# Optimization experiments

Measured on AMD Instinct MI355X. Metric: run time of the kernel, lower is better.

The kernel has to match this reference:

```python
import jax, jax.numpy as jnp
import jax.scipy.fft as jsp_fft
import numpy as np

B, NX, NY, DV = 4, 512, 512, 32
KX, KY = 64, 64


def setup_inputs() -> dict:
    key = jax.random.key(0)
    k1, k2, k3 = jax.random.split(key, 3)
    x = jax.random.normal(k1, (B, NX, NY, DV), dtype=jnp.float32)
    R_real = jax.random.uniform(k2, (DV, DV, KX, KY), dtype=jnp.float32)
    R_imag = jax.random.uniform(k3, (DV, DV, KX, KY), dtype=jnp.float32)
    return {"x": x, "R_real": R_real, "R_imag": R_imag}


def reference(x, R_real, R_imag):
    # x: [B, nX, nY, dv]
    R = R_real + 1j * R_imag  # [dv_out, dv_in, kX, kY]
    kX, kY = R.shape[-2:]
    nX = x.shape[1]

    xt = jnp.moveaxis(x, -1, -3)                      # [B, dv, nX, nY]
    xd = jsp_fft.dct(xt, type=2, axis=-1, norm='ortho')   # DCT-II along Y
    xf = jnp.fft.rfft(xd, axis=-2, norm='ortho')      # [B, dv, nX//2+1, nY] complex
    nXf, nY = xf.shape[-2:]

    # Truncation einsum with identity-padded T matrices == slicing
    xtr = xf[..., :kX, :kY]                           # [B, dv, kX, kY]
    # Per-mode complex channel mixing
    y = jnp.einsum('ijab,ejab->eiab', R, xtr)         # [B, dv, kX, kY]
    # Inverse truncation == zero-padding back to full spectrum
    yp = jnp.pad(y, ((0, 0), (0, 0), (0, nXf - kX), (0, nY - kY)))

    yr = jnp.fft.irfft(yp, n=nX, axis=-2, norm='ortho')
    yd = jsp_fft.idct(yr, type=2, axis=-1, norm='ortho')
    return jnp.moveaxis(yd, -3, -1)                   # [B, nX, nY, dv]
```

## Files before the change

kernel.cpp:

```cpp
#include <hip/hip_runtime.h>
#include <math.h>

#define BB 4
#define NXD 512
#define NYD 512
#define DVD 32
#define KXD 64
#define KYD 64

#define OFF_DN  0
#define OFF_DT  32768
#define OFF_FCN 65536
#define OFF_FSN 98304
#define OFF_FCT 131072
#define OFF_FST 163840
#define OFF_C   196608
#define OFF_FR  4390912
#define OFF_FI  4915200
#define OFF_YR  5439488
#define OFF_YI  5963776
#define OFF_G   6488064

__global__ __launch_bounds__(256) void k_tables(float* __restrict__ ws) {
    int idx = blockIdx.x * 256 + threadIdx.x;
    int k = idx >> 9;
    int n = idx & 511;
    const float inv_sq512 = 0.04419417382415922f;
    float ak = (k == 0) ? inv_sq512 : 0.0625f;
    int m = (k * (2 * n + 1)) & 2047;
    float d = ak * cospif((float)m * (1.0f / 1024.0f));
    ws[OFF_DN + k * 512 + n] = d;
    ws[OFF_DT + n * 64 + k] = d;
    int mf = (k * n) & 511;
    float c = cospif((float)mf * (1.0f / 256.0f)) * inv_sq512;
    float s = sinpif((float)mf * (1.0f / 256.0f)) * inv_sq512;
    ws[OFF_FCN + k * 512 + n] = c;
    ws[OFF_FSN + k * 512 + n] = s;
    ws[OFF_FCT + n * 64 + k] = c;
    ws[OFF_FST + n * 64 + k] = s;
}

__global__ __launch_bounds__(256) void k_dct(const float* __restrict__ x,
                                             const float* __restrict__ ws,
                                             float* __restrict__ C) {
    __shared__ __align__(16) float xs[2][64 * 32];
    __shared__ __align__(16) float dt[64 * 64];
    int b = blockIdx.x >> 8;
    int nx = (blockIdx.x & 255) * 2;
    int t = threadIdx.x;
    int dv0 = (t & 15) * 2;
    int ky0 = (t >> 4) * 4;
    const float* Dt = ws + OFF_DT;
    float a[2][4][2] = {};
    for (int ch = 0; ch < 8; ++ch) {
        int ny0 = ch * 64;
        __syncthreads();
#pragma unroll
        for (int n = 0; n < 2; ++n) {
            const float4* src = (const float4*)(x + ((size_t)(b * NXD + nx + n) * NYD + ny0) * DVD);
            float4* dst = (float4*)xs[n];
#pragma unroll
            for (int p = 0; p < 2; ++p) dst[p * 256 + t] = src[p * 256 + t];
        }
        {
            const float4* src = (const float4*)(Dt + ny0 * 64);
            float4* dst = (float4*)dt;
#pragma unroll
            for (int p = 0; p < 4; ++p) dst[p * 256 + t] = src[p * 256 + t];
        }
        __syncthreads();
#pragma unroll 4
        for (int nyc = 0; nyc < 64; ++nyc) {
            float4 d4 = *(const float4*)(dt + nyc * 64 + ky0);
            float2 x0 = *(const float2*)(xs[0] + nyc * 32 + dv0);
            float2 x1 = *(const float2*)(xs[1] + nyc * 32 + dv0);
            float da[4] = {d4.x, d4.y, d4.z, d4.w};
#pragma unroll
            for (int q = 0; q < 4; ++q) {
                a[0][q][0] += da[q] * x0.x; a[0][q][1] += da[q] * x0.y;
                a[1][q][0] += da[q] * x1.x; a[1][q][1] += da[q] * x1.y;
            }
        }
    }
#pragma unroll
    for (int n = 0; n < 2; ++n)
#pragma unroll
        for (int q = 0; q < 4; ++q) {
            float2 v; v.x = a[n][q][0]; v.y = a[n][q][1];
            *(float2*)(C + ((size_t)((b * KYD + ky0 + q) * NXD + nx + n)) * DVD + dv0) = v;
        }
}

__global__ __launch_bounds__(256) void k_rfft(const float* __restrict__ Cbuf,
                                              const float* __restrict__ ws,
                                              float* __restrict__ Fr,
                                              float* __restrict__ Fi) {
    __shared__ __align__(16) float cs[256 * 16];
    int b = blockIdx.x >> 7;
    int r = blockIdx.x & 127;
    int ky = r >> 1;
    int dvbase = (r & 1) * 16;
    int t = threadIdx.x;
    int dv0 = (t & 7) * 2;
    int kx0 = (t >> 3) * 2;
    const float* Tc = ws + OFF_FCT;
    const float* Ts = ws + OFF_FST;
    float ar[2][2] = {}, ai[2][2] = {};
    for (int ch = 0; ch < 2; ++ch) {
        int nx0 = ch * 256;
        __syncthreads();
#pragma unroll
        for (int p = 0; p < 4; ++p) {
            int fi4 = p * 256 + t;
            int row = fi4 >> 2, c4 = fi4 & 3;
            *(float4*)(cs + row * 16 + c4 * 4) =
                *(const float4*)(Cbuf + ((size_t)(b * KYD + ky) * NXD + nx0 + row) * DVD + dvbase + c4 * 4);
        }
        __syncthreads();
#pragma unroll 4
        for (int nxc = 0; nxc < 256; ++nxc) {
            float2 cv = *(const float2*)(cs + nxc * 16 + dv0);
            float2 c2 = *(const float2*)(Tc + (nx0 + nxc) * 64 + kx0);
            float2 s2 = *(const float2*)(Ts + (nx0 + nxc) * 64 + kx0);
            ar[0][0] += c2.x * cv.x; ar[0][1] += c2.x * cv.y;
            ar[1][0] += c2.y * cv.x; ar[1][1] += c2.y * cv.y;
            ai[0][0] -= s2.x * cv.x; ai[0][1] -= s2.x * cv.y;
            ai[1][0] -= s2.y * cv.x; ai[1][1] -= s2.y * cv.y;
        }
    }
#pragma unroll
    for (int q = 0; q < 2; ++q) {
        size_t o = ((size_t)((b * KYD + ky) * KXD + kx0 + q)) * DVD + dvbase + dv0;
        float2 vr; vr.x = ar[q][0]; vr.y = ar[q][1];
        float2 vi; vi.x = ai[q][0]; vi.y = ai[q][1];
        *(float2*)(Fr + o) = vr;
        *(float2*)(Fi + o) = vi;
    }
}

__global__ __launch_bounds__(256) void k_mix(const float* __restrict__ Rr,
                                             const float* __restrict__ Ri,
                                             const float* __restrict__ Fr,
                                             const float* __restrict__ Fi,
                                             float* __restrict__ Yr,
                                             float* __restrict__ Yi) {
    __shared__ float fl[4 * 32 * 64 * 2];
    int kx = blockIdx.x & 63;
    int ig = blockIdx.x >> 6;
    int t = threadIdx.x;
    int j = t & 31, kyb = t >> 5;
#pragma unroll
    for (int e = 0; e < 4; ++e) {
#pragma unroll
        for (int p = 0; p < 8; ++p) {
            int ky = p * 8 + kyb;
            size_t go = ((size_t)((e * KYD + ky) * KXD + kx)) * DVD + j;
            int lo = ((e * 32 + j) * 64 + ((ky + j) & 63)) * 2;
            fl[lo] = Fr[go];
            fl[lo + 1] = Fi[go];
        }
    }
    __syncthreads();
    int lane = t & 63, w = t >> 6;
    int i = ig * 4 + w;
    float yr[4] = {}, yi[4] = {};
    for (int jj = 0; jj < 32; ++jj) {
        float rr = Rr[(((size_t)i * 32 + jj) * 64 + kx) * 64 + lane];
        float ri = Ri[(((size_t)i * 32 + jj) * 64 + kx) * 64 + lane];
#pragma unroll
        for (int e = 0; e < 4; ++e) {
            float2 f = *(const float2*)(fl + ((e * 32 + jj) * 64 + ((lane + jj) & 63)) * 2);
            yr[e] += rr * f.x - ri * f.y;
            yi[e] += rr * f.y + ri * f.x;
        }
    }
#pragma unroll
    for (int e = 0; e < 4; ++e) {
        size_t o = ((size_t)((e * DVD + i) * KXD + kx)) * KYD + lane;
        Yr[o] = yr[e];
        Yi[o] = yi[e];
    }
}

__global__ __launch_bounds__(256) void k_irfft(const float* __restrict__ Yr,
                                               const float* __restrict__ Yi,
                                               const float* __restrict__ ws,
                                               float* __restrict__ G) {
    __shared__ __align__(16) float ylr[64 * 64];
    __shared__ __align__(16) float yli[64 * 64];
    int blk = blockIdx.x;
    int oct = blk & 7;
    int i = (blk >> 3) & 31;
    int b = blk >> 8;
    int t = threadIdx.x;
    size_t ybase = ((size_t)(b * DVD + i)) * KXD * KYD;
#pragma unroll
    for (int p = 0; p < 16; ++p) {
        int idx = p * 256 + t;
        float wk = (idx < 64) ? 1.0f : 2.0f;
        ylr[idx] = Yr[ybase + idx] * wk;
        yli[idx] = Yi[ybase + idx] * wk;
    }
    __syncthreads();
    int kyg = t & 15, nxg = t >> 4;
    int ky0 = kyg * 4;
    int gnx0 = oct * 64 + nxg * 4;
    const float* Tc = ws + OFF_FCN;
    const float* Ts = ws + OFF_FSN;
    float acc[4][4] = {};
    for (int kx = 0; kx < 64; ++kx) {
        float4 cv = *(const float4*)(Tc + kx * 512 + gnx0);
        float4 sv = *(const float4*)(Ts + kx * 512 + gnx0);
        float4 vr = *(const float4*)(ylr + kx * 64 + ky0);
        float4 vi = *(const float4*)(yli + kx * 64 + ky0);
        float ca[4] = {cv.x, cv.y, cv.z, cv.w};
        float sa[4] = {sv.x, sv.y, sv.z, sv.w};
        float ra[4] = {vr.x, vr.y, vr.z, vr.w};
        float ia[4] = {vi.x, vi.y, vi.z, vi.w};
#pragma unroll
        for (int q = 0; q < 4; ++q)
#pragma unroll
            for (int kk = 0; kk < 4; ++kk)
                acc[q][kk] += ca[q] * ra[kk] - sa[q] * ia[kk];
    }
#pragma unroll
    for (int q = 0; q < 4; ++q) {
        float4 v; v.x = acc[q][0]; v.y = acc[q][1]; v.z = acc[q][2]; v.w = acc[q][3];
        *(float4*)(G + (((size_t)(b * NXD + gnx0 + q)) * DVD + i) * KYD + ky0) = v;
    }
}

#define GST 68
__global__ __launch_bounds__(256) void k_idct(const float* __restrict__ G,
                                              const float* __restrict__ ws,
                                              float* __restrict__ out) {
    __shared__ __align__(16) float gs[2][32 * GST];
    __shared__ __align__(16) float dn[64 * 64];
    int b = blockIdx.x >> 8;
    int nx = (blockIdx.x & 255) * 2;
    int t = threadIdx.x;
    int ig = t & 15, nyg = t >> 4;
    int i0 = ig * 2;
    const float* Dn = ws + OFF_DN;
#pragma unroll
    for (int n = 0; n < 2; ++n) {
        const float4* src = (const float4*)(G + (size_t)(b * NXD + nx + n) * DVD * KYD);
#pragma unroll
        for (int p = 0; p < 2; ++p) {
            int f = p * 256 + t;
            int i = f >> 4, ky4 = (f & 15) * 4;
            *(float4*)(gs[n] + i * GST + ky4) = src[f];
        }
    }
    float* outb = out + ((size_t)(b * NXD + nx)) * NYD * DVD;
    for (int c = 0; c < 8; ++c) {
        __syncthreads();
        {
            float4* dst = (float4*)dn;
#pragma unroll
            for (int p = 0; p < 4; ++p) {
                int f = p * 256 + t;
                int ky = f >> 4, ny4 = (f & 15) * 4;
                dst[f] = *(const float4*)(Dn + ky * 512 + c * 64 + ny4);
            }
        }
        __syncthreads();
        float acc[2][4][2] = {};
#pragma unroll 2
        for (int kyc = 0; kyc < 16; ++kyc) {
            int ky0 = kyc * 4;
            float4 g00 = *(const float4*)(gs[0] + i0 * GST + ky0);
            float4 g01 = *(const float4*)(gs[0] + (i0 + 1) * GST + ky0);
            float4 g10 = *(const float4*)(gs[1] + i0 * GST + ky0);
            float4 g11 = *(const float4*)(gs[1] + (i0 + 1) * GST + ky0);
            float g0a[2][4] = {{g00.x, g00.y, g00.z, g00.w}, {g10.x, g10.y, g10.z, g10.w}};
            float g1a[2][4] = {{g01.x, g01.y, g01.z, g01.w}, {g11.x, g11.y, g11.z, g11.w}};
#pragma unroll
            for (int kk = 0; kk < 4; ++kk) {
                float4 dv = *(const float4*)(dn + (ky0 + kk) * 64 + nyg * 4);
                float da[4] = {dv.x, dv.y, dv.z, dv.w};
#pragma unroll
                for (int q = 0; q < 4; ++q) {
                    acc[0][q][0] += da[q] * g0a[0][kk];
                    acc[0][q][1] += da[q] * g1a[0][kk];
                    acc[1][q][0] += da[q] * g0a[1][kk];
                    acc[1][q][1] += da[q] * g1a[1][kk];
                }
            }
        }
        int ny0 = c * 64 + nyg * 4;
#pragma unroll
        for (int n = 0; n < 2; ++n)
#pragma unroll
            for (int q = 0; q < 4; ++q) {
                float2 v; v.x = acc[n][q][0]; v.y = acc[n][q][1];
                *(float2*)(outb + ((size_t)n * NYD + ny0 + q) * DVD + i0) = v;
            }
    }
}

extern "C" void kernel_launch(void* const* d_in, const int* in_sizes, int n_in,
                              void* d_out, int out_size, void* d_ws, size_t ws_size,
                              hipStream_t stream) {
    const float* x  = (const float*)d_in[0];
    const float* Rr = (const float*)d_in[1];
    const float* Ri = (const float*)d_in[2];
    float* out = (float*)d_out;
    float* ws  = (float*)d_ws;
    float* C   = ws + OFF_C;
    float* Fr  = ws + OFF_FR;
    float* Fi  = ws + OFF_FI;
    float* Yr  = ws + OFF_YR;
    float* Yi  = ws + OFF_YI;
    float* G   = ws + OFF_G;

    k_tables<<<128, 256, 0, stream>>>(ws);
    k_dct<<<BB * (NXD / 2), 256, 0, stream>>>(x, ws, C);
    k_rfft<<<BB * KYD * 2, 256, 0, stream>>>(C, ws, Fr, Fi);
    k_mix<<<KXD * 8, 256, 0, stream>>>(Rr, Ri, Fr, Fi, Yr, Yi);
    k_irfft<<<BB * DVD * 8, 256, 0, stream>>>(Yr, Yi, ws, G);
    k_idct<<<BB * NXD / 2, 256, 0, stream>>>(G, ws, out);
}
```

Before: 432.1 us.

## Double-buffer DCT/rFFT staging with direct global-to-LDS loads and retune other kernels

In the DCT and rFFT kernels, x and C tiles are now staged into shared memory with direct global-to-LDS loads into two buffers, so the next chunk loads while the current one is computed. The DCT and iDCT kernels also stop copying the cosine tables into shared memory and read them straight from global memory (cache). The mixing kernel is split across twice as many blocks, each handling two batches, to raise parallelism. The irFFT kernel loads its input with float4 accesses. The risks are more global or cache traffic for the table reads, twice the R reads in the mixing kernel, and correctness of the asynchronous LDS loads without explicit waits beyond the barriers.

After: 469.3 us. 1.09x slower.

```diff
diff --git a/kernel.cpp b/kernel.cpp
--- a/kernel.cpp
+++ b/kernel.cpp
@@ -20,6 +20,12 @@
 #define OFF_YR  5439488
 #define OFF_YI  5963776
 #define OFF_G   6488064
+
+__device__ __forceinline__ void gload_lds16(const float* g, float* l) {
+    __builtin_amdgcn_global_load_lds(
+        (const __attribute__((address_space(1))) void*)g,
+        (__attribute__((address_space(3))) void*)l, 16, 0, 0);
+}
 
 __global__ __launch_bounds__(256) void k_tables(float* __restrict__ ws) {
     int idx = blockIdx.x * 256 + threadIdx.x;
@@ -43,37 +49,41 @@
 __global__ __launch_bounds__(256) void k_dct(const float* __restrict__ x,
                                              const float* __restrict__ ws,
                                              float* __restrict__ C) {
-    __shared__ __align__(16) float xs[2][64 * 32];
-    __shared__ __align__(16) float dt[64 * 64];
+    __shared__ __align__(16) float xs[2][2 * 2048];
     int b = blockIdx.x >> 8;
     int nx = (blockIdx.x & 255) * 2;
     int t = threadIdx.x;
+    int wv = t >> 6;
     int dv0 = (t & 15) * 2;
     int ky0 = (t >> 4) * 4;
     const float* Dt = ws + OFF_DT;
+    const float* xb = x + (size_t)(b * NXD + nx) * NYD * DVD;
+
+    auto stage = [&](int buf, int ch) {
+#pragma unroll
+        for (int n = 0; n < 2; ++n) {
+            const float* src = xb + ((size_t)n * NYD + ch * 64) * DVD;
+#pragma unroll
+            for (int p = 0; p < 2; ++p) {
+                int f = p * 256 + t;
+                gload_lds16(src + f * 4, xs[buf] + n * 2048 + (p * 256 + wv * 64) * 4);
+            }
+        }
+    };
+
     float a[2][4][2] = {};
+    stage(0, 0);
+    __syncthreads();
     for (int ch = 0; ch < 8; ++ch) {
-        int ny0 = ch * 64;
-        __syncthreads();
-#pragma unroll
-        for (int n = 0; n < 2; ++n) {
-            const float4* src = (const float4*)(x + ((size_t)(b * NXD + nx + n) * NYD + ny0) * DVD);
-            float4* dst = (float4*)xs[n];
-#pragma unroll
-            for (int p = 0; p < 2; ++p) dst[p * 256 + t] = src[p * 256 + t];
-        }
-        {
-            const float4* src = (const float4*)(Dt + ny0 * 64);
-            float4* dst = (float4*)dt;
-#pragma unroll
-            for (int p = 0; p < 4; ++p) dst[p * 256 + t] = src[p * 256 + t];
-        }
-        __syncthreads();
+        int buf = ch & 1;
+        if (ch < 7) stage(buf ^ 1, ch + 1);
+        const float* dtc = Dt + ch * 4096 + ky0;
+        const float* xsb = xs[buf];
 #pragma unroll 4
         for (int nyc = 0; nyc < 64; ++nyc) {
-            float4 d4 = *(const float4*)(dt + nyc * 64 + ky0);
-            float2 x0 = *(const float2*)(xs[0] + nyc * 32 + dv0);
-            float2 x1 = *(const float2*)(xs[1] + nyc * 32 + dv0);
+            float4 d4 = *(const float4*)(dtc + nyc * 64);
+            float2 x0 = *(const float2*)(xsb + nyc * 32 + dv0);
+            float2 x1 = *(const float2*)(xsb + 2048 + nyc * 32 + dv0);
             float da[4] = {d4.x, d4.y, d4.z, d4.w};
 #pragma unroll
             for (int q = 0; q < 4; ++q) {
@@ -81,6 +91,7 @@
                 a[1][q][0] += da[q] * x1.x; a[1][q][1] += da[q] * x1.y;
             }
         }
+        __syncthreads();
     }
 #pragma unroll
     for (int n = 0; n < 2; ++n)
@@ -95,31 +106,39 @@
                                               const float* __restrict__ ws,
                                               float* __restrict__ Fr,
                                               float* __restrict__ Fi) {
-    __shared__ __align__(16) float cs[256 * 16];
+    __shared__ __align__(16) float cs[2][4096];
     int b = blockIdx.x >> 7;
     int r = blockIdx.x & 127;
     int ky = r >> 1;
     int dvbase = (r & 1) * 16;
     int t = threadIdx.x;
+    int wv = t >> 6;
     int dv0 = (t & 7) * 2;
     int kx0 = (t >> 3) * 2;
     const float* Tc = ws + OFF_FCT;
     const float* Ts = ws + OFF_FST;
-    float ar[2][2] = {}, ai[2][2] = {};
-    for (int ch = 0; ch < 2; ++ch) {
-        int nx0 = ch * 256;
-        __syncthreads();
+    const float* Cb = Cbuf + (size_t)(b * KYD + ky) * NXD * DVD + dvbase;
+
+    auto stage = [&](int buf, int ch) {
 #pragma unroll
         for (int p = 0; p < 4; ++p) {
             int fi4 = p * 256 + t;
             int row = fi4 >> 2, c4 = fi4 & 3;
-            *(float4*)(cs + row * 16 + c4 * 4) =
-                *(const float4*)(Cbuf + ((size_t)(b * KYD + ky) * NXD + nx0 + row) * DVD + dvbase + c4 * 4);
-        }
-        __syncthreads();
-#pragma unroll 4
+            gload_lds16(Cb + (size_t)(ch * 256 + row) * DVD + c4 * 4,
+                        cs[buf] + (p * 256 + wv * 64) * 4);
+        }
+    };
+
+    float ar[2][2] = {}, ai[2][2] = {};
+    stage(0, 0);
+    __syncthreads();
+    for (int ch = 0; ch < 2; ++ch) {
+        if (ch == 0) stage(1, 1);
+        const float* csb = cs[ch];
+        int nx0 = ch * 256;
+#pragma unroll 8
         for (int nxc = 0; nxc < 256; ++nxc) {
-            float2 cv = *(const float2*)(cs + nxc * 16 + dv0);
+            float2 cv = *(const float2*)(csb + nxc * 16 + dv0);
             float2 c2 = *(const float2*)(Tc + (nx0 + nxc) * 64 + kx0);
             float2 s2 = *(const float2*)(Ts + (nx0 + nxc) * 64 + kx0);
             ar[0][0] += c2.x * cv.x; ar[0][1] += c2.x * cv.y;
@@ -127,6 +146,7 @@
             ai[0][0] -= s2.x * cv.x; ai[0][1] -= s2.x * cv.y;
             ai[1][0] -= s2.y * cv.x; ai[1][1] -= s2.y * cv.y;
         }
+        __syncthreads();
     }
 #pragma unroll
     for (int q = 0; q < 2; ++q) {
@@ -144,18 +164,20 @@
                                              const float* __restrict__ Fi,
                                              float* __restrict__ Yr,
                                              float* __restrict__ Yi) {
-    __shared__ float fl[4 * 32 * 64 * 2];
+    __shared__ float fl[2 * 32 * 64 * 2];
     int kx = blockIdx.x & 63;
-    int ig = blockIdx.x >> 6;
+    int ig = (blockIdx.x >> 6) & 7;
+    int eh = blockIdx.x >> 9;
     int t = threadIdx.x;
     int j = t & 31, kyb = t >> 5;
 #pragma unroll
-    for (int e = 0; e < 4; ++e) {
+    for (int e2 = 0; e2 < 2; ++e2) {
+        int e = eh * 2 + e2;
 #pragma unroll
         for (int p = 0; p < 8; ++p) {
             int ky = p * 8 + kyb;
             size_t go = ((size_t)((e * KYD + ky) * KXD + kx)) * DVD + j;
-            int lo = ((e * 32 + j) * 64 + ((ky + j) & 63)) * 2;
+            int lo = ((e2 * 32 + j) * 64 + ((ky + j) & 63)) * 2;
             fl[lo] = Fr[go];
             fl[lo + 1] = Fi[go];
         }
@@ -163,22 +185,25 @@
     __syncthreads();
     int lane = t & 63, w = t >> 6;
     int i = ig * 4 + w;
-    float yr[4] = {}, yi[4] = {};
+    size_t rb = (size_t)(i * 32) * 4096 + kx * 64 + lane;
+    float yr[2] = {}, yi[2] = {};
+#pragma unroll 8
     for (int jj = 0; jj < 32; ++jj) {
-        float rr = Rr[(((size_t)i * 32 + jj) * 64 + kx) * 64 + lane];
-        float ri = Ri[(((size_t)i * 32 + jj) * 64 + kx) * 64 + lane];
-#pragma unroll
-        for (int e = 0; e < 4; ++e) {
-            float2 f = *(const float2*)(fl + ((e * 32 + jj) * 64 + ((lane + jj) & 63)) * 2);
-            yr[e] += rr * f.x - ri * f.y;
-            yi[e] += rr * f.y + ri * f.x;
-        }
-    }
-#pragma unroll
-    for (int e = 0; e < 4; ++e) {
+        float rr = Rr[rb + (size_t)jj * 4096];
+        float ri = Ri[rb + (size_t)jj * 4096];
+#pragma unroll
+        for (int e2 = 0; e2 < 2; ++e2) {
+            float2 f = *(const float2*)(fl + ((e2 * 32 + jj) * 64 + ((lane + jj) & 63)) * 2);
+            yr[e2] += rr * f.x - ri * f.y;
+            yi[e2] += rr * f.y + ri * f.x;
+        }
+    }
+#pragma unroll
+    for (int e2 = 0; e2 < 2; ++e2) {
+        int e = eh * 2 + e2;
         size_t o = ((size_t)((e * DVD + i) * KXD + kx)) * KYD + lane;
-        Yr[o] = yr[e];
-        Yi[o] = yi[e];
+        Yr[o] = yr[e2];
+        Yi[o] = yi[e2];
     }
 }
 
@@ -195,11 +220,15 @@
     int t = threadIdx.x;
     size_t ybase = ((size_t)(b * DVD + i)) * KXD * KYD;
 #pragma unroll
-    for (int p = 0; p < 16; ++p) {
-        int idx = p * 256 + t;
-        float wk = (idx < 64) ? 1.0f : 2.0f;
-        ylr[idx] = Yr[ybase + idx] * wk;
-        yli[idx] = Yi[ybase + idx] * wk;
+    for (int p = 0; p < 4; ++p) {
+        int f = p * 256 + t;
+        float wk = (f < 16) ? 1.0f : 2.0f;
+        float4 vr = *(const float4*)(Yr + ybase + (size_t)f * 4);
+        float4 vi = *(const float4*)(Yi + ybase + (size_t)f * 4);
+        vr.x *= wk; vr.y *= wk; vr.z *= wk; vr.w *= wk;
+        vi.x *= wk; vi.y *= wk; vi.z *= wk; vi.w *= wk;
+        *(float4*)(ylr + f * 4) = vr;
+        *(float4*)(yli + f * 4) = vi;
     }
     __syncthreads();
     int kyg = t & 15, nxg = t >> 4;
@@ -235,7 +264,6 @@
                                               const float* __restrict__ ws,
                                               float* __restrict__ out) {
     __shared__ __align__(16) float gs[2][32 * GST];
-    __shared__ __align__(16) float dn[64 * 64];
     int b = blockIdx.x >> 8;
     int nx = (blockIdx.x & 255) * 2;
     int t = threadIdx.x;
@@ -252,19 +280,10 @@
             *(float4*)(gs[n] + i * GST + ky4) = src[f];
         }
     }
+    __syncthreads();
     float* outb = out + ((size_t)(b * NXD + nx)) * NYD * DVD;
     for (int c = 0; c < 8; ++c) {
-        __syncthreads();
-        {
-            float4* dst = (float4*)dn;
-#pragma unroll
-            for (int p = 0; p < 4; ++p) {
-                int f = p * 256 + t;
-                int ky = f >> 4, ny4 = (f & 15) * 4;
-                dst[f] = *(const float4*)(Dn + ky * 512 + c * 64 + ny4);
-            }
-        }
-        __syncthreads();
+        const float* dnc = Dn + c * 64 + nyg * 4;
         float acc[2][4][2] = {};
 #pragma unroll 2
         for (int kyc = 0; kyc < 16; ++kyc) {
@@ -277,7 +296,7 @@
             float g1a[2][4] = {{g01.x, g01.y, g01.z, g01.w}, {g11.x, g11.y, g11.z, g11.w}};
 #pragma unroll
             for (int kk = 0; kk < 4; ++kk) {
-                float4 dv = *(const float4*)(dn + (ky0 + kk) * 64 + nyg * 4);
+                float4 dv = *(const float4*)(dnc + (ky0 + kk) * 512);
                 float da[4] = {dv.x, dv.y, dv.z, dv.w};
 #pragma unroll
                 for (int q = 0; q < 4; ++q) {
@@ -317,7 +336,7 @@
     k_tables<<<128, 256, 0, stream>>>(ws);
     k_dct<<<BB * (NXD / 2), 256, 0, stream>>>(x, ws, C);
     k_rfft<<<BB * KYD * 2, 256, 0, stream>>>(C, ws, Fr, Fi);
-    k_mix<<<KXD * 8, 256, 0, stream>>>(Rr, Ri, Fr, Fi, Yr, Yi);
+    k_mix<<<KXD * 8 * 2, 256, 0, stream>>>(Rr, Ri, Fr, Fi, Yr, Yi);
     k_irfft<<<BB * DVD * 8, 256, 0, stream>>>(Yr, Yi, ws, G);
     k_idct<<<BB * NXD / 2, 256, 0, stream>>>(G, ws, out);
 }
```
